# Kernel optimization log

Measured on AMD Instinct MI355X. Metric: run time of the kernel, lower is better.

Reference implementation:

```python
import jax, jax.numpy as jnp
import numpy as np

B, N, D, P, K = 4, 2048, 512, 16, 4
EPS_BW = 1e-8
EPS_LN = 1e-5


def setup_inputs() -> dict:
    key = jax.random.key(0)
    ks = jax.random.split(key, 8)
    charge = jax.random.normal(ks[0], (B, N, D), dtype=jnp.float32)
    position = jax.random.normal(ks[1], (B, N, P), dtype=jnp.float32)
    mass = jax.random.uniform(ks[2], (B, N, 1), dtype=jnp.float32)
    # parameters
    log_bandwidth = jnp.zeros((K,), dtype=jnp.float32)
    W_charge = jax.random.normal(ks[3], (D * K, D), dtype=jnp.float32) / np.sqrt(D)   # torch Linear weight (out,in)
    W_combine = jax.random.normal(ks[4], (D, D * K), dtype=jnp.float32) / np.sqrt(D * K)
    gamma = jnp.ones((D,), dtype=jnp.float32)
    beta = jnp.zeros((D,), dtype=jnp.float32)
    return {"charge": charge, "position": position, "mass": mass,
            "log_bandwidth": log_bandwidth, "W_charge": W_charge,
            "W_combine": W_combine, "gamma": gamma, "beta": beta}


def reference(charge, position, mass, log_bandwidth, W_charge, W_combine, gamma, beta):
    # pairwise squared distances: (B, N, N)
    diff = position[:, :, None, :] - position[:, None, :, :]
    dist_sq = jnp.sum(diff * diff, axis=-1)
    # multi-bandwidth Gaussian kernels: (B, N, N, K)
    bandwidths = jnp.exp(log_bandwidth)
    kernels = jnp.exp(-dist_sq[..., None] / (2.0 * bandwidths + EPS_BW))
    # mass weighting: mass (B,N,1) -> (B,1,N,1), broadcast over query axis and kernels
    weighted_kernels = kernels * mass[:, None, :, :]
    # project charges: (B, N, K, D)
    projected = (charge @ W_charge.T).reshape(B, N, K, D)
    # aggregate over neighbours j: field[b,i,k,d] = sum_j wk[b,i,j,k] * proj[b,j,k,d]
    field = jnp.einsum('bijk,bjkd->bikd', weighted_kernels, projected)
    field = field.reshape(B, N, K * D) @ W_combine.T  # (B, N, D)
    # LayerNorm
    mean = jnp.mean(field, axis=-1, keepdims=True)
    var = jnp.var(field, axis=-1, keepdims=True)
    normed = (field - mean) * jax.lax.rsqrt(var + EPS_LN)
    return normed * gamma + beta
```

## Files before the change

### kernel.cpp

```cpp
#include <hip/hip_runtime.h>


typedef __bf16 bf16x8 __attribute__((ext_vector_type(8)));
typedef float f32x4 __attribute__((ext_vector_type(4)));

__device__ __forceinline__ unsigned short f2bf(float f) {
    unsigned u = __float_as_uint(f);
    unsigned r = (u + 0x7fffu + ((u >> 16) & 1u)) >> 16;
    return (unsigned short)r;
}
__device__ __forceinline__ float bf2f(unsigned short h) {
    return __uint_as_float(((unsigned)h) << 16);
}
__device__ __forceinline__ void g2l16(const unsigned short* g, unsigned short* l) {
    __builtin_amdgcn_global_load_lds(
        (const __attribute__((address_space(1))) unsigned int*)g,
        (__attribute__((address_space(3))) unsigned int*)l, 16, 0, 0);
}

__global__ __launch_bounds__(256) void k0_pos(const float* __restrict__ pos,
                                              unsigned short* __restrict__ posA,
                                              unsigned short* __restrict__ posB1,
                                              unsigned short* __restrict__ posB2,
                                              float* __restrict__ rsq)
{
    const int row = blockIdx.x * 256 + threadIdx.x;
    const float* src = &pos[(size_t)row * 16];
    float p[16];
#pragma unroll
    for (int cc = 0; cc < 4; cc++) {
        float4 v = *reinterpret_cast<const float4*>(&src[cc * 4]);
        p[cc * 4 + 0] = v.x; p[cc * 4 + 1] = v.y; p[cc * 4 + 2] = v.z; p[cc * 4 + 3] = v.w;
    }
    float r = 0.f;
    unsigned short h[16], lo[16], z[8] = {0, 0, 0, 0, 0, 0, 0, 0};
#pragma unroll
    for (int d = 0; d < 16; d++) {
        r = __builtin_fmaf(p[d], p[d], r);
        h[d] = f2bf(p[d]);
        lo[d] = f2bf(p[d] - bf2f(h[d]));
    }
    rsq[row] = r;
    size_t o = (size_t)row * 32;
    *reinterpret_cast<int4*>(&posA[o + 0])   = *reinterpret_cast<int4*>(&h[0]);
    *reinterpret_cast<int4*>(&posA[o + 8])   = *reinterpret_cast<int4*>(&h[8]);
    *reinterpret_cast<int4*>(&posA[o + 16])  = *reinterpret_cast<int4*>(&lo[0]);
    *reinterpret_cast<int4*>(&posA[o + 24])  = *reinterpret_cast<int4*>(&lo[8]);
    *reinterpret_cast<int4*>(&posB1[o + 0])  = *reinterpret_cast<int4*>(&h[0]);
    *reinterpret_cast<int4*>(&posB1[o + 8])  = *reinterpret_cast<int4*>(&h[8]);
    *reinterpret_cast<int4*>(&posB1[o + 16]) = *reinterpret_cast<int4*>(&h[0]);
    *reinterpret_cast<int4*>(&posB1[o + 24]) = *reinterpret_cast<int4*>(&h[8]);
    *reinterpret_cast<int4*>(&posB2[o + 0])  = *reinterpret_cast<int4*>(&lo[0]);
    *reinterpret_cast<int4*>(&posB2[o + 8])  = *reinterpret_cast<int4*>(&lo[8]);
    *reinterpret_cast<int4*>(&posB2[o + 16]) = *reinterpret_cast<int4*>(&z[0]);
    *reinterpret_cast<int4*>(&posB2[o + 24]) = *reinterpret_cast<int4*>(&z[0]);
}

__global__ __launch_bounds__(256) void k0_cvt(const float* __restrict__ src,
                                              unsigned short* __restrict__ dst)
{
    size_t i = (size_t)blockIdx.x * 256 + threadIdx.x;
    float4 v = reinterpret_cast<const float4*>(src)[i];
    unsigned short o[4] = {f2bf(v.x), f2bf(v.y), f2bf(v.z), f2bf(v.w)};
    reinterpret_cast<uint2*>(dst)[i] = *reinterpret_cast<uint2*>(&o[0]);
}

__global__ __launch_bounds__(256, 2) void k1_proj(const unsigned short* __restrict__ wc16,
                                                  const unsigned short* __restrict__ ch16,
                                                  const float* __restrict__ mass,
                                                  unsigned short* __restrict__ projm_t)
{
    __shared__ alignas(16) unsigned short As[128 * 32];
    __shared__ alignas(16) unsigned short Bs[128 * 32];
    const int tid = threadIdx.x, lane = tid & 63, wid = tid >> 6;
    const int q = lane >> 4, l15 = lane & 15;
    const int m0 = blockIdx.y * 128, n0 = blockIdx.x * 128;
    const int wm = (wid & 1) * 64, wn = (wid >> 1) * 64;

    f32x4 acc[4][4];
#pragma unroll
    for (int i = 0; i < 4; i++)
#pragma unroll
        for (int j = 0; j < 4; j++) acc[i][j] = (f32x4){0.f, 0.f, 0.f, 0.f};

    for (int k0 = 0; k0 < 512; k0 += 32) {
        __syncthreads();
#pragma unroll
        for (int q4 = 0; q4 < 4; q4++) {
            int chunk = q4 * 256 + tid;
            int w = chunk & 511, row = w >> 2, c4 = w & 3;
            if (chunk < 512)
                g2l16(&wc16[(size_t)(m0 + row) * 512 + k0 + c4 * 8], &As[w * 8]);
            else
                g2l16(&ch16[(size_t)(n0 + row) * 512 + k0 + c4 * 8], &Bs[w * 8]);
        }
        __syncthreads();
        bf16x8 af[4], bfr[4];
#pragma unroll
        for (int it = 0; it < 4; it++)
            af[it] = *reinterpret_cast<const bf16x8*>(&As[(wm + it * 16 + l15) * 32 + q * 8]);
#pragma unroll
        for (int ct = 0; ct < 4; ct++)
            bfr[ct] = *reinterpret_cast<const bf16x8*>(&Bs[(wn + ct * 16 + l15) * 32 + q * 8]);
#pragma unroll
        for (int it = 0; it < 4; it++)
#pragma unroll
            for (int ct = 0; ct < 4; ct++)
                acc[it][ct] = __builtin_amdgcn_mfma_f32_16x16x32_bf16(af[it], bfr[ct], acc[it][ct], 0, 0, 0);
    }
#pragma unroll
    for (int ct = 0; ct < 4; ct++) {
        int n = n0 + wn + ct * 16 + l15;
        float mf = mass[n];
#pragma unroll
        for (int it = 0; it < 4; it++) {
            int mrow = m0 + wm + it * 16 + q * 4;
#pragma unroll
            for (int r = 0; r < 4; r++)
                projm_t[(size_t)(mrow + r) * 8192 + n] = f2bf(acc[it][ct][r] * mf);
        }
    }
}

__global__ __launch_bounds__(256, 2) void k2_field(const unsigned short* __restrict__ posA,
                                                   const unsigned short* __restrict__ posB1,
                                                   const unsigned short* __restrict__ posB2,
                                                   const float* __restrict__ rsq,
                                                   const float* __restrict__ logbw,
                                                   const unsigned short* __restrict__ projm_t,
                                                   unsigned short* __restrict__ field)
{
    __shared__ alignas(16) unsigned short Bs[2][256 * 32];
    __shared__ alignas(16) unsigned short pB1[2][32 * 32];
    __shared__ alignas(16) unsigned short pB2[2][32 * 32];
    __shared__ alignas(16) unsigned short Wl[2][64 * 40];

    const int tid = threadIdx.x, lane = tid & 63, wid = tid >> 6;
    const int q = lane >> 4, l15 = lane & 15;
    const int b = blockIdx.z, i0 = blockIdx.x * 64, c0 = blockIdx.y * 256;
    const int kb = c0 >> 9;
    const float bw = __expf(logbw[kb]);
    const float s2 = -1.4426950408889634f / (2.0f * bw + 1e-8f);
    const float c2 = -2.0f * s2;

    const bf16x8 afG = *reinterpret_cast<const bf16x8*>(
        &posA[(size_t)(b * 2048 + i0 + wid * 16 + l15) * 32 + q * 8]);
    float riv[4];
#pragma unroll
    for (int r = 0; r < 4; r++) riv[r] = rsq[b * 2048 + i0 + wid * 16 + q * 4 + r];

    f32x4 acc[4][4];
#pragma unroll
    for (int i = 0; i < 4; i++)
#pragma unroll
        for (int j = 0; j < 4; j++) acc[i][j] = (f32x4){0.f, 0.f, 0.f, 0.f};

    for (int j0 = 0; j0 < 2048; j0 += 64) {
        __syncthreads();
        {
            const size_t gb = (size_t)c0 * 8192 + b * 2048 + j0;
#pragma unroll
            for (int q8 = 0; q8 < 8; q8++) {
                int chunk = q8 * 256 + tid;
                int s = chunk >> 10, w1 = chunk & 1023;
                g2l16(&projm_t[gb + (size_t)(w1 >> 2) * 8192 + s * 32 + (w1 & 3) * 8],
                      &Bs[s][w1 * 8]);
            }
        }
        {
            const size_t gp = (size_t)(b * 2048 + j0) * 32;
#pragma unroll
            for (int q2 = 0; q2 < 2; q2++) {
                int chunk = q2 * 256 + tid;
                int w = chunk & 255, s = w >> 7, w2 = w & 127;
                if (chunk < 256)
                    g2l16(&posB1[gp + s * 1024 + w2 * 8], &pB1[s][w2 * 8]);
                else
                    g2l16(&posB2[gp + s * 1024 + w2 * 8], &pB2[s][w2 * 8]);
            }
        }
        __syncthreads();
#pragma unroll
        for (int s = 0; s < 2; s++) {
#pragma unroll
            for (int jt2 = 0; jt2 < 2; jt2++) {
                bf16x8 b2 = *reinterpret_cast<const bf16x8*>(&pB2[s][(jt2 * 16 + l15) * 32 + q * 8]);
                bf16x8 b1 = *reinterpret_cast<const bf16x8*>(&pB1[s][(jt2 * 16 + l15) * 32 + q * 8]);
                f32x4 g = (f32x4){0.f, 0.f, 0.f, 0.f};
                g = __builtin_amdgcn_mfma_f32_16x16x32_bf16(afG, b2, g, 0, 0, 0);
                g = __builtin_amdgcn_mfma_f32_16x16x32_bf16(afG, b1, g, 0, 0, 0);
                int j = s * 32 + jt2 * 16 + l15;
                float rj = rsq[b * 2048 + j0 + j];
#pragma unroll
                for (int r = 0; r < 4; r++) {
                    float x = __builtin_fmaf(g[r], c2, (riv[r] + rj) * s2);
                    Wl[s][(wid * 16 + q * 4 + r) * 40 + (jt2 * 16 + l15)] =
                        f2bf(__builtin_amdgcn_exp2f(x));
                }
            }
        }
        __syncthreads();
#pragma unroll
        for (int s = 0; s < 2; s++) {
            bf16x8 af[4], bfr[4];
#pragma unroll
            for (int it = 0; it < 4; it++)
                af[it] = *reinterpret_cast<const bf16x8*>(&Wl[s][(it * 16 + l15) * 40 + q * 8]);
#pragma unroll
            for (int ct = 0; ct < 4; ct++)
                bfr[ct] = *reinterpret_cast<const bf16x8*>(&Bs[s][(wid * 64 + ct * 16 + l15) * 32 + q * 8]);
#pragma unroll
            for (int it = 0; it < 4; it++)
#pragma unroll
                for (int ct = 0; ct < 4; ct++)
                    acc[it][ct] = __builtin_amdgcn_mfma_f32_16x16x32_bf16(af[it], bfr[ct], acc[it][ct], 0, 0, 0);
        }
    }
#pragma unroll
    for (int it = 0; it < 4; it++) {
#pragma unroll
        for (int ct = 0; ct < 4; ct++) {
            int gi = b * 2048 + i0 + it * 16 + q * 4;
            int gc = c0 + wid * 64 + ct * 16 + l15;
#pragma unroll
            for (int r = 0; r < 4; r++)
                field[(size_t)(gi + r) * 2048 + gc] = f2bf(acc[it][ct][r]);
        }
    }
}

__global__ __launch_bounds__(256, 2) void k3_combine(const unsigned short* __restrict__ field,
                                                     const unsigned short* __restrict__ wcb16,
                                                     float* __restrict__ out)
{
    __shared__ alignas(16) unsigned short As[128 * 32];
    __shared__ alignas(16) unsigned short Bs[64 * 32];
    const int tid = threadIdx.x, lane = tid & 63, wid = tid >> 6;
    const int q = lane >> 4, l15 = lane & 15;
    const int m0 = blockIdx.y * 128, n0 = blockIdx.x * 64;
    const int wm = wid * 32;

    f32x4 acc[2][4];
#pragma unroll
    for (int i = 0; i < 2; i++)
#pragma unroll
        for (int j = 0; j < 4; j++) acc[i][j] = (f32x4){0.f, 0.f, 0.f, 0.f};

    for (int k0 = 0; k0 < 2048; k0 += 32) {
        __syncthreads();
#pragma unroll
        for (int q3 = 0; q3 < 3; q3++) {
            int chunk = q3 * 256 + tid;
            if (chunk < 512) {
                int row = chunk >> 2, c4 = chunk & 3;
                g2l16(&field[(size_t)(m0 + row) * 2048 + k0 + c4 * 8], &As[chunk * 8]);
            } else {
                int w = chunk - 512, row = w >> 2, c4 = w & 3;
                g2l16(&wcb16[(size_t)(n0 + row) * 2048 + k0 + c4 * 8], &Bs[w * 8]);
            }
        }
        __syncthreads();
        bf16x8 af[2], bfr[4];
#pragma unroll
        for (int it = 0; it < 2; it++)
            af[it] = *reinterpret_cast<const bf16x8*>(&As[(wm + it * 16 + l15) * 32 + q * 8]);
#pragma unroll
        for (int ct = 0; ct < 4; ct++)
            bfr[ct] = *reinterpret_cast<const bf16x8*>(&Bs[(ct * 16 + l15) * 32 + q * 8]);
#pragma unroll
        for (int it = 0; it < 2; it++)
#pragma unroll
            for (int ct = 0; ct < 4; ct++)
                acc[it][ct] = __builtin_amdgcn_mfma_f32_16x16x32_bf16(af[it], bfr[ct], acc[it][ct], 0, 0, 0);
    }
#pragma unroll
    for (int it = 0; it < 2; it++) {
#pragma unroll
        for (int ct = 0; ct < 4; ct++) {
            int m = m0 + wm + it * 16 + q * 4;
            int n = n0 + ct * 16 + l15;
#pragma unroll
            for (int r = 0; r < 4; r++)
                out[(size_t)(m + r) * 512 + n] = acc[it][ct][r];
        }
    }
}

__global__ __launch_bounds__(256) void k4_ln(float* __restrict__ out,
                                             const float* __restrict__ gamma,
                                             const float* __restrict__ beta)
{
    __shared__ float red[8];
    const int row = blockIdx.x, tid = threadIdx.x;
    float2 x = *reinterpret_cast<const float2*>(&out[(size_t)row * 512 + tid * 2]);
    float s = x.x + x.y;
    float ss = x.x * x.x + x.y * x.y;
#pragma unroll
    for (int off = 32; off > 0; off >>= 1) {
        s += __shfl_down(s, off);
        ss += __shfl_down(ss, off);
    }
    int wid = tid >> 6;
    if ((tid & 63) == 0) { red[wid * 2] = s; red[wid * 2 + 1] = ss; }
    __syncthreads();
    s = red[0] + red[2] + red[4] + red[6];
    ss = red[1] + red[3] + red[5] + red[7];
    float mean = s * (1.f / 512.f);
    float var = ss * (1.f / 512.f) - mean * mean;
    float inv = rsqrtf(var + 1e-5f);
    float g0 = gamma[tid * 2], g1 = gamma[tid * 2 + 1];
    float b0 = beta[tid * 2], b1 = beta[tid * 2 + 1];
    float2 o;
    o.x = (x.x - mean) * inv * g0 + b0;
    o.y = (x.y - mean) * inv * g1 + b1;
    *reinterpret_cast<float2*>(&out[(size_t)row * 512 + tid * 2]) = o;
}

extern "C" void kernel_launch(void* const* d_in, const int* in_sizes, int n_in,
                              void* d_out, int out_size, void* d_ws, size_t ws_size,
                              hipStream_t stream)
{
    const float* charge   = (const float*)d_in[0];
    const float* position = (const float*)d_in[1];
    const float* mass     = (const float*)d_in[2];
    const float* logbw    = (const float*)d_in[3];
    const float* Wc       = (const float*)d_in[4];
    const float* Wcb      = (const float*)d_in[5];
    const float* gamma    = (const float*)d_in[6];
    const float* beta     = (const float*)d_in[7];

    unsigned short* projm_t = (unsigned short*)d_ws;
    unsigned short* field   = projm_t + (size_t)2048 * 8192;
    unsigned short* wcb16   = projm_t;
    unsigned short* ch16    = field;
    unsigned short* wc16    = field + (size_t)8192 * 512;
    unsigned short* posA  = (unsigned short*)d_out;
    unsigned short* posB1 = posA + (size_t)8192 * 32;
    unsigned short* posB2 = posB1 + (size_t)8192 * 32;
    float* rsq = (float*)(posB2 + (size_t)8192 * 32);
    float* out = (float*)d_out;

    k0_pos<<<32, 256, 0, stream>>>(position, posA, posB1, posB2, rsq);
    k0_cvt<<<4096, 256, 0, stream>>>(charge, ch16);
    k0_cvt<<<1024, 256, 0, stream>>>(Wc, wc16);
    k1_proj<<<dim3(64, 16), 256, 0, stream>>>(wc16, ch16, mass, projm_t);
    k2_field<<<dim3(32, 8, 4), 256, 0, stream>>>(posA, posB1, posB2, rsq, logbw, projm_t, field);
    k0_cvt<<<1024, 256, 0, stream>>>(Wcb, wcb16);
    k3_combine<<<dim3(8, 64), 256, 0, stream>>>(field, wcb16, out);
    k4_ln<<<8192, 256, 0, stream>>>(out, gamma, beta);
}
```

Before: 300.8 us.

## Enlarge field tile to 128 rows with XCD-aware block mapping, reshape combine tiles

```diff
diff --git a/kernel.cpp b/kernel.cpp
--- a/kernel.cpp
+++ b/kernel.cpp
@@ -133,29 +133,47 @@
     __shared__ alignas(16) unsigned short Bs[2][256 * 32];
     __shared__ alignas(16) unsigned short pB1[2][32 * 32];
     __shared__ alignas(16) unsigned short pB2[2][32 * 32];
-    __shared__ alignas(16) unsigned short Wl[2][64 * 40];
+    __shared__ alignas(16) unsigned short Wl[2][128 * 40];
 
     const int tid = threadIdx.x, lane = tid & 63, wid = tid >> 6;
     const int q = lane >> 4, l15 = lane & 15;
-    const int b = blockIdx.z, i0 = blockIdx.x * 64, c0 = blockIdx.y * 256;
+    const int L = blockIdx.x;
+    const int xcd = L & 7, idx = L >> 3;
+    const int i_t = idx & 15, cb = xcd * 4 + (idx >> 4);
+    const int c0 = (cb & 7) * 256, b = cb >> 3;
+    const int i0 = i_t * 128;
     const int kb = c0 >> 9;
     const float bw = __expf(logbw[kb]);
     const float s2 = -1.4426950408889634f / (2.0f * bw + 1e-8f);
     const float c2 = -2.0f * s2;
 
-    const bf16x8 afG = *reinterpret_cast<const bf16x8*>(
-        &posA[(size_t)(b * 2048 + i0 + wid * 16 + l15) * 32 + q * 8]);
-    float riv[4];
-#pragma unroll
-    for (int r = 0; r < 4; r++) riv[r] = rsq[b * 2048 + i0 + wid * 16 + q * 4 + r];
-
-    f32x4 acc[4][4];
+    bf16x8 afG[2];
+    float riv[2][4];
+#pragma unroll
+    for (int t = 0; t < 2; t++) {
+        afG[t] = *reinterpret_cast<const bf16x8*>(
+            &posA[(size_t)(b * 2048 + i0 + wid * 32 + t * 16 + l15) * 32 + q * 8]);
+#pragma unroll
+        for (int r = 0; r < 4; r++)
+            riv[t][r] = rsq[b * 2048 + i0 + wid * 32 + t * 16 + q * 4 + r];
+    }
+
+    const int wo_i = (wid >> 1) * 64, wo_c = (wid & 1) * 128;
+
+    f32x4 acc[4][8];
 #pragma unroll
     for (int i = 0; i < 4; i++)
 #pragma unroll
-        for (int j = 0; j < 4; j++) acc[i][j] = (f32x4){0.f, 0.f, 0.f, 0.f};
+        for (int j = 0; j < 8; j++) acc[i][j] = (f32x4){0.f, 0.f, 0.f, 0.f};
 
     for (int j0 = 0; j0 < 2048; j0 += 64) {
+        float rjv[2][2];
+#pragma unroll
+        for (int s = 0; s < 2; s++)
+#pragma unroll
+            for (int jt2 = 0; jt2 < 2; jt2++)
+                rjv[s][jt2] = rsq[b * 2048 + j0 + s * 32 + jt2 * 16 + l15];
+
         __syncthreads();
         {
             const size_t gb = (size_t)c0 * 8192 + b * 2048 + j0;
@@ -186,42 +204,44 @@
             for (int jt2 = 0; jt2 < 2; jt2++) {
                 bf16x8 b2 = *reinterpret_cast<const bf16x8*>(&pB2[s][(jt2 * 16 + l15) * 32 + q * 8]);
                 bf16x8 b1 = *reinterpret_cast<const bf16x8*>(&pB1[s][(jt2 * 16 + l15) * 32 + q * 8]);
-                f32x4 g = (f32x4){0.f, 0.f, 0.f, 0.f};
-                g = __builtin_amdgcn_mfma_f32_16x16x32_bf16(afG, b2, g, 0, 0, 0);
-                g = __builtin_amdgcn_mfma_f32_16x16x32_bf16(afG, b1, g, 0, 0, 0);
-                int j = s * 32 + jt2 * 16 + l15;
-                float rj = rsq[b * 2048 + j0 + j];
-#pragma unroll
-                for (int r = 0; r < 4; r++) {
-                    float x = __builtin_fmaf(g[r], c2, (riv[r] + rj) * s2);
-                    Wl[s][(wid * 16 + q * 4 + r) * 40 + (jt2 * 16 + l15)] =
-                        f2bf(__builtin_amdgcn_exp2f(x));
+#pragma unroll
+                for (int t = 0; t < 2; t++) {
+                    f32x4 g = (f32x4){0.f, 0.f, 0.f, 0.f};
+                    g = __builtin_amdgcn_mfma_f32_16x16x32_bf16(afG[t], b2, g, 0, 0, 0);
+                    g = __builtin_amdgcn_mfma_f32_16x16x32_bf16(afG[t], b1, g, 0, 0, 0);
+                    float rj = rjv[s][jt2];
+#pragma unroll
+                    for (int r = 0; r < 4; r++) {
+                        float x = __builtin_fmaf(g[r], c2, (riv[t][r] + rj) * s2);
+                        Wl[s][(wid * 32 + t * 16 + q * 4 + r) * 40 + (jt2 * 16 + l15)] =
+                            f2bf(__builtin_amdgcn_exp2f(x));
+                    }
                 }
             }
         }
         __syncthreads();
 #pragma unroll
         for (int s = 0; s < 2; s++) {
-            bf16x8 af[4], bfr[4];
+            bf16x8 af[4], bfr[8];
 #pragma unroll
             for (int it = 0; it < 4; it++)
-                af[it] = *reinterpret_cast<const bf16x8*>(&Wl[s][(it * 16 + l15) * 40 + q * 8]);
-#pragma unroll
-            for (int ct = 0; ct < 4; ct++)
-                bfr[ct] = *reinterpret_cast<const bf16x8*>(&Bs[s][(wid * 64 + ct * 16 + l15) * 32 + q * 8]);
+                af[it] = *reinterpret_cast<const bf16x8*>(&Wl[s][(wo_i + it * 16 + l15) * 40 + q * 8]);
+#pragma unroll
+            for (int ct = 0; ct < 8; ct++)
+                bfr[ct] = *reinterpret_cast<const bf16x8*>(&Bs[s][(wo_c + ct * 16 + l15) * 32 + q * 8]);
 #pragma unroll
             for (int it = 0; it < 4; it++)
 #pragma unroll
-                for (int ct = 0; ct < 4; ct++)
+                for (int ct = 0; ct < 8; ct++)
                     acc[it][ct] = __builtin_amdgcn_mfma_f32_16x16x32_bf16(af[it], bfr[ct], acc[it][ct], 0, 0, 0);
         }
     }
 #pragma unroll
     for (int it = 0; it < 4; it++) {
 #pragma unroll
-        for (int ct = 0; ct < 4; ct++) {
-            int gi = b * 2048 + i0 + it * 16 + q * 4;
-            int gc = c0 + wid * 64 + ct * 16 + l15;
+        for (int ct = 0; ct < 8; ct++) {
+            int gi = b * 2048 + i0 + wo_i + it * 16 + q * 4;
+            int gc = c0 + wo_c + ct * 16 + l15;
 #pragma unroll
             for (int r = 0; r < 4; r++)
                 field[(size_t)(gi + r) * 2048 + gc] = f2bf(acc[it][ct][r]);
@@ -233,52 +253,52 @@
                                                      const unsigned short* __restrict__ wcb16,
                                                      float* __restrict__ out)
 {
-    __shared__ alignas(16) unsigned short As[128 * 32];
-    __shared__ alignas(16) unsigned short Bs[64 * 32];
+    __shared__ alignas(16) unsigned short As[64 * 32];
+    __shared__ alignas(16) unsigned short Bs[128 * 32];
     const int tid = threadIdx.x, lane = tid & 63, wid = tid >> 6;
     const int q = lane >> 4, l15 = lane & 15;
-    const int m0 = blockIdx.y * 128, n0 = blockIdx.x * 64;
-    const int wm = wid * 32;
-
-    f32x4 acc[2][4];
-#pragma unroll
-    for (int i = 0; i < 2; i++)
-#pragma unroll
-        for (int j = 0; j < 4; j++) acc[i][j] = (f32x4){0.f, 0.f, 0.f, 0.f};
+    const int m0 = blockIdx.y * 64, n0 = blockIdx.x * 128;
+    const int wn = wid * 32;
+
+    f32x4 acc[4][2];
+#pragma unroll
+    for (int i = 0; i < 4; i++)
+#pragma unroll
+        for (int j = 0; j < 2; j++) acc[i][j] = (f32x4){0.f, 0.f, 0.f, 0.f};
 
     for (int k0 = 0; k0 < 2048; k0 += 32) {
         __syncthreads();
 #pragma unroll
         for (int q3 = 0; q3 < 3; q3++) {
             int chunk = q3 * 256 + tid;
-            if (chunk < 512) {
+            if (chunk < 256) {
                 int row = chunk >> 2, c4 = chunk & 3;
                 g2l16(&field[(size_t)(m0 + row) * 2048 + k0 + c4 * 8], &As[chunk * 8]);
             } else {
-                int w = chunk - 512, row = w >> 2, c4 = w & 3;
+                int w = chunk - 256, row = w >> 2, c4 = w & 3;
                 g2l16(&wcb16[(size_t)(n0 + row) * 2048 + k0 + c4 * 8], &Bs[w * 8]);
             }
         }
         __syncthreads();
-        bf16x8 af[2], bfr[4];
-#pragma unroll
-        for (int it = 0; it < 2; it++)
-            af[it] = *reinterpret_cast<const bf16x8*>(&As[(wm + it * 16 + l15) * 32 + q * 8]);
-#pragma unroll
-        for (int ct = 0; ct < 4; ct++)
-            bfr[ct] = *reinterpret_cast<const bf16x8*>(&Bs[(ct * 16 + l15) * 32 + q * 8]);
-#pragma unroll
-        for (int it = 0; it < 2; it++)
-#pragma unroll
-            for (int ct = 0; ct < 4; ct++)
+        bf16x8 af[4], bfr[2];
+#pragma unroll
+        for (int it = 0; it < 4; it++)
+            af[it] = *reinterpret_cast<const bf16x8*>(&As[(it * 16 + l15) * 32 + q * 8]);
+#pragma unroll
+        for (int ct = 0; ct < 2; ct++)
+            bfr[ct] = *reinterpret_cast<const bf16x8*>(&Bs[(wn + ct * 16 + l15) * 32 + q * 8]);
+#pragma unroll
+        for (int it = 0; it < 4; it++)
+#pragma unroll
+            for (int ct = 0; ct < 2; ct++)
                 acc[it][ct] = __builtin_amdgcn_mfma_f32_16x16x32_bf16(af[it], bfr[ct], acc[it][ct], 0, 0, 0);
     }
 #pragma unroll
-    for (int it = 0; it < 2; it++) {
-#pragma unroll
-        for (int ct = 0; ct < 4; ct++) {
-            int m = m0 + wm + it * 16 + q * 4;
-            int n = n0 + ct * 16 + l15;
+    for (int it = 0; it < 4; it++) {
+#pragma unroll
+        for (int ct = 0; ct < 2; ct++) {
+            int m = m0 + it * 16 + q * 4;
+            int n = n0 + wn + ct * 16 + l15;
 #pragma unroll
             for (int r = 0; r < 4; r++)
                 out[(size_t)(m + r) * 512 + n] = acc[it][ct][r];
@@ -344,8 +364,8 @@
     k0_cvt<<<4096, 256, 0, stream>>>(charge, ch16);
     k0_cvt<<<1024, 256, 0, stream>>>(Wc, wc16);
     k1_proj<<<dim3(64, 16), 256, 0, stream>>>(wc16, ch16, mass, projm_t);
-    k2_field<<<dim3(32, 8, 4), 256, 0, stream>>>(posA, posB1, posB2, rsq, logbw, projm_t, field);
+    k2_field<<<512, 256, 0, stream>>>(posA, posB1, posB2, rsq, logbw, projm_t, field);
     k0_cvt<<<1024, 256, 0, stream>>>(Wcb, wcb16);
-    k3_combine<<<dim3(8, 64), 256, 0, stream>>>(field, wcb16, out);
+    k3_combine<<<dim3(4, 128), 256, 0, stream>>>(field, wcb16, out);
     k4_ln<<<8192, 256, 0, stream>>>(out, gamma, beta);
 }
```

Measured after the change: 263.2 us. 1.14x faster.
